# Performance work log

Hardware: AMD Instinct MI355X
Metric: run time of the kernel (lower is better)

Reference implementation:

```python
import jax, jax.numpy as jnp
import numpy as np

BS, T, H = 4, 2048, 512
N_HEAD = 8
D_HEAD = H // N_HEAD  # 64


def setup_inputs() -> dict:
    key = jax.random.key(0)
    k1, k2, k3 = jax.random.split(key, 3)
    x = jax.random.normal(k1, (BS, T, H), dtype=jnp.float32)
    # torch Linear(hidden, (2*n_head+1)*d_head) -> store transposed for x @ W
    w_qkv = jax.random.normal(k2, (H, (2 * N_HEAD + 1) * D_HEAD), dtype=jnp.float32) * (H ** -0.5)
    w_out = jax.random.normal(k3, (D_HEAD, H), dtype=jnp.float32) * (D_HEAD ** -0.5)
    return {"x": x, "w_qkv": w_qkv, "w_out": w_out}


def reference(x, w_qkv, w_out):
    bs, t, h = x.shape
    n_head, d_head = N_HEAD, D_HEAD
    scale = d_head ** -0.5

    qkv = x @ w_qkv  # [bs, t, (2*n_head+1)*d_head]
    q, k, v = jnp.split(qkv, [n_head * d_head, 2 * n_head * d_head], axis=-1)
    q = q.reshape(bs, t, n_head, d_head)
    k = k.reshape(bs, t, n_head, d_head)
    # v stays [bs, t, d_head]: a single V shared across all heads

    # causal mask: -inf strictly above the diagonal
    mask = jnp.triu(jnp.full((t, t), -jnp.inf, dtype=x.dtype), 1)

    # scores: [bs, n_head, t_q, t_k]
    attn_score = jnp.einsum('bqhd,bkhd->bhqk', q, k) * scale + mask
    attn_prob = jax.nn.softmax(attn_score, axis=-1)

    # shared V broadcast over heads: [bs, n_head, t, d_head]
    attn_vec = jnp.einsum('bhqk,bkd->bhqd', attn_prob, v)
    m_attn_vec = jnp.mean(attn_vec, axis=1)  # mean over heads -> [bs, t, d_head]

    out = m_attn_vec @ w_out  # [bs, t, hidden]
    return out, attn_prob
```

## Files before the change

### kernel.cpp

```cpp
#include <hip/hip_runtime.h>

typedef unsigned short u16;
typedef __bf16 bf16x8 __attribute__((ext_vector_type(8)));
typedef float f32x4 __attribute__((ext_vector_type(4)));
static_assert(sizeof(bf16x8) == 16, "bf16x8 must be 16B");

#define MFMA(a, b, c) __builtin_amdgcn_mfma_f32_16x16x32_bf16(a, b, c, 0, 0, 0)

__device__ __forceinline__ u16 f2bf(float f) {
  unsigned u = __float_as_uint(f);
  u += 0x7fffu + ((u >> 16) & 1u);
  return (u16)(u >> 16);
}

__global__ __launch_bounds__(256) void prep_kernel(
    const float* __restrict__ x, const float* __restrict__ wqkv,
    const float* __restrict__ wout, u16* __restrict__ xh,
    u16* __restrict__ wt, u16* __restrict__ wot) {
  int blk = blockIdx.x, tid = threadIdx.x;
  if (blk < 4096) {
    int idx = (blk * 256 + tid) * 4;
    float4 v = *(const float4*)(x + idx);
    ushort4 o;
    o.x = f2bf(v.x); o.y = f2bf(v.y); o.z = f2bf(v.z); o.w = f2bf(v.w);
    *(ushort4*)(xh + idx) = o;
  } else if (blk < 4096 + 2176) {
    int idx = (blk - 4096) * 256 + tid;
    int n = idx >> 9, k = idx & 511;
    float v = wqkv[k * 1088 + n];
    if (n < 512) v *= 0.125f;
    wt[idx] = f2bf(v);
  } else {
    int idx = (blk - 6272) * 256 + tid;
    int n = idx >> 6, d = idx & 63;
    wot[idx] = f2bf(wout[d * 512 + n]);
  }
}

__global__ __launch_bounds__(256) void qkv_gemm_kernel(
    const u16* __restrict__ xh, const u16* __restrict__ wt,
    u16* __restrict__ Qb, u16* __restrict__ Kb, u16* __restrict__ Vt) {
  __shared__ u16 As[128][40];
  __shared__ u16 Bs[64][40];
  const int tid = threadIdx.x;
  const int w = tid >> 6, l = tid & 63, g = l >> 4, c16 = l & 15;
  const int n0 = blockIdx.x * 64;
  const int m0 = blockIdx.y * 128;
  const int arow = tid >> 1, acol = (tid & 1) << 4;
  const int brow = tid >> 2, bcol = (tid & 3) << 3;
  const u16* ap = xh + (size_t)(m0 + arow) * 512 + acol;
  const u16* bp = wt + (size_t)(n0 + brow) * 512 + bcol;
  uint4 pa0 = *(const uint4*)(ap);
  uint4 pa1 = *(const uint4*)(ap + 8);
  uint4 pb0 = *(const uint4*)(bp);
  f32x4 acc[2][4] = {};
  for (int k0 = 0; k0 < 512; k0 += 32) {
    __syncthreads();
    *(uint4*)&As[arow][acol] = pa0;
    *(uint4*)&As[arow][acol + 8] = pa1;
    *(uint4*)&Bs[brow][bcol] = pb0;
    __syncthreads();
    if (k0 + 32 < 512) {
      pa0 = *(const uint4*)(ap + k0 + 32);
      pa1 = *(const uint4*)(ap + k0 + 40);
      pb0 = *(const uint4*)(bp + k0 + 32);
    }
#pragma unroll
    for (int mt = 0; mt < 2; ++mt) {
      bf16x8 a = *(const bf16x8*)&As[w * 32 + mt * 16 + c16][g * 8];
#pragma unroll
      for (int nt = 0; nt < 4; ++nt) {
        bf16x8 b = *(const bf16x8*)&Bs[nt * 16 + c16][g * 8];
        acc[mt][nt] = MFMA(a, b, acc[mt][nt]);
      }
    }
  }
#pragma unroll
  for (int mt = 0; mt < 2; ++mt)
#pragma unroll
    for (int nt = 0; nt < 4; ++nt)
#pragma unroll
      for (int j = 0; j < 4; ++j) {
        u16 bv = f2bf(acc[mt][nt][j]);
        int row = m0 + w * 32 + mt * 16 + g * 4 + j;
        int b = row >> 11, t = row & 2047;
        int col = n0 + nt * 16 + c16;
        if (col < 512) {
          int h = col >> 6, d = col & 63;
          Qb[((size_t)((b << 3) + h) * 2048 + t) * 64 + d] = bv;
        } else if (col < 1024) {
          int cc = col - 512, h = cc >> 6, d = cc & 63;
          Kb[((size_t)((b << 3) + h) * 2048 + t) * 64 + d] = bv;
        } else {
          int d = col - 1024;
          Vt[((size_t)((b << 6) + d)) * 2048 + t] = bv;
        }
      }
}

__global__ __launch_bounds__(256, 4) void attn_kernel(
    const u16* __restrict__ Qb, const u16* __restrict__ Kb,
    const u16* __restrict__ Vt, float* __restrict__ P,
    float* __restrict__ Obuf) {
  __shared__ u16 Ps[64][72];
  const int tid = threadIdx.x;
  const int w = tid >> 6, l = tid & 63, g = l >> 4, c16 = l & 15;
  const int bidx = blockIdx.x;
  const int ii = bidx >> 5, jj = bidx & 31;
  const int qt = ((ii >> 3) & 1) ? (31 - jj) : jj;
  const int bh = ii, b = bh >> 3;

  const u16* qrow = Qb + ((size_t)(bh * 2048 + qt * 64 + w * 16 + c16)) * 64;
  const bf16x8 aq0 = *(const bf16x8*)(qrow + g * 8);
  const bf16x8 aq1 = *(const bf16x8*)(qrow + 32 + g * 8);

  const u16* kb = Kb + ((size_t)bh * 2048) * 64;
  const u16* vb = Vt + ((size_t)(b << 6)) * 2048;

  float lsum = 0.f;

  for (int kt = 0; kt <= qt; ++kt) {
    const u16* kp = kb + (size_t)kt * 4096;
    f32x4 st[4];
    __builtin_amdgcn_s_setprio(1);
#pragma unroll
    for (int nt = 0; nt < 4; ++nt) {
      const u16* kr = kp + (size_t)(nt * 16 + c16) * 64 + g * 8;
      bf16x8 k0 = *(const bf16x8*)(kr);
      bf16x8 k1 = *(const bf16x8*)(kr + 32);
      f32x4 a = {};
      a = MFMA(k0, aq0, a);
      a = MFMA(k1, aq1, a);
      st[nt] = a;
    }
    __builtin_amdgcn_s_setprio(0);
    if (kt == qt) {
#pragma unroll
      for (int nt = 0; nt < 4; ++nt)
#pragma unroll
        for (int j = 0; j < 4; ++j)
          if (nt * 16 + g * 4 + j > w * 16 + c16) st[nt][j] = -3.0e38f;
    }
#pragma unroll
    for (int nt = 0; nt < 4; ++nt)
#pragma unroll
      for (int j = 0; j < 4; ++j) lsum += __expf(st[nt][j]);
  }
  lsum += __shfl_xor(lsum, 16, 64);
  lsum += __shfl_xor(lsum, 32, 64);
  const float rl = 1.0f / lsum;

  f32x4 oacc[4] = {};
  float* prow = P +
      ((size_t)(bh * 2048 + qt * 64 + w * 16 + c16)) * 2048 + g * 4;
  for (int kt = 0; kt <= qt; ++kt) {
    const u16* kp = kb + (size_t)kt * 4096;
    f32x4 st[4];
    __builtin_amdgcn_s_setprio(1);
#pragma unroll
    for (int nt = 0; nt < 4; ++nt) {
      const u16* kr = kp + (size_t)(nt * 16 + c16) * 64 + g * 8;
      bf16x8 k0 = *(const bf16x8*)(kr);
      bf16x8 k1 = *(const bf16x8*)(kr + 32);
      f32x4 a = {};
      a = MFMA(k0, aq0, a);
      a = MFMA(k1, aq1, a);
      st[nt] = a;
    }
    __builtin_amdgcn_s_setprio(0);
    if (kt == qt) {
#pragma unroll
      for (int nt = 0; nt < 4; ++nt)
#pragma unroll
        for (int j = 0; j < 4; ++j)
          if (nt * 16 + g * 4 + j > w * 16 + c16) st[nt][j] = -3.0e38f;
    }
#pragma unroll
    for (int nt = 0; nt < 4; ++nt) {
      f32x4 pv;
#pragma unroll
      for (int j = 0; j < 4; ++j) pv[j] = __expf(st[nt][j]) * rl;
      __builtin_nontemporal_store(
          pv, (f32x4*)(prow + (size_t)kt * 64 + nt * 16));
      unsigned r0, r1;
      asm("v_cvt_pk_bf16_f32 %0, %1, %2" : "=v"(r0) : "v"(pv[0]), "v"(pv[1]));
      asm("v_cvt_pk_bf16_f32 %0, %1, %2" : "=v"(r1) : "v"(pv[2]), "v"(pv[3]));
      uint2 pk; pk.x = r0; pk.y = r1;
      *(uint2*)&Ps[w * 16 + c16][nt * 16 + g * 4] = pk;
    }
    bf16x8 ap0 = *(const bf16x8*)&Ps[w * 16 + c16][g * 8];
    bf16x8 ap1 = *(const bf16x8*)&Ps[w * 16 + c16][32 + g * 8];
    __builtin_amdgcn_s_setprio(1);
#pragma unroll
    for (int nt = 0; nt < 4; ++nt) {
      const u16* vr = vb + (size_t)(nt * 16 + c16) * 2048 + kt * 64 + g * 8;
      bf16x8 v0 = *(const bf16x8*)(vr);
      bf16x8 v1 = *(const bf16x8*)(vr + 32);
      oacc[nt] = MFMA(ap0, v0, oacc[nt]);
      oacc[nt] = MFMA(ap1, v1, oacc[nt]);
    }
    __builtin_amdgcn_s_setprio(0);
  }

  {
    float* obase = Obuf + ((size_t)(bh * 2048 + qt * 64 + w * 16)) * 64;
#pragma unroll
    for (int nt = 0; nt < 4; ++nt)
#pragma unroll
      for (int j = 0; j < 4; ++j)
        obase[(g * 4 + j) * 64 + nt * 16 + c16] = oacc[nt][j];
  }
  {
    int colstart = (qt + 1) * 64;
    int nf4 = (2048 - colstart) >> 2;
    float* base = P + ((size_t)(bh * 2048 + qt * 64)) * 2048;
    f32x4 z = {0.f, 0.f, 0.f, 0.f};
    for (int r = 0; r < 64; ++r) {
      f32x4* rowp = (f32x4*)(base + (size_t)r * 2048 + colstart);
      for (int u = tid; u < nf4; u += 256)
        __builtin_nontemporal_store(z, rowp + u);
    }
  }
}

__global__ __launch_bounds__(256) void mean_kernel(
    const float* __restrict__ Obuf, u16* __restrict__ meanb) {
  int o4 = blockIdx.x * 256 + threadIdx.x;
  int d4 = o4 & 15, t = (o4 >> 4) & 2047, b = o4 >> 15;
  f32x4 acc = {0.f, 0.f, 0.f, 0.f};
#pragma unroll
  for (int h = 0; h < 8; ++h) {
    f32x4 v = *(const f32x4*)(Obuf +
        ((size_t)((b << 3) + h) * 2048 + t) * 64 + d4 * 4);
    acc += v;
  }
  ushort4 o;
  o.x = f2bf(acc[0] * 0.125f); o.y = f2bf(acc[1] * 0.125f);
  o.z = f2bf(acc[2] * 0.125f); o.w = f2bf(acc[3] * 0.125f);
  *(ushort4*)(meanb + (size_t)o4 * 4) = o;
}

__global__ __launch_bounds__(256) void out_gemm_kernel(
    const u16* __restrict__ meanb, const u16* __restrict__ wot,
    float* __restrict__ out) {
  __shared__ u16 As[64][72];
  __shared__ u16 Bs[64][72];
  const int tid = threadIdx.x;
  const int w = tid >> 6, l = tid & 63, g = l >> 4, c16 = l & 15;
  const int n0 = blockIdx.x * 64;
  const int m0 = blockIdx.y * 64;
  const int srow = tid >> 2, scol = (tid & 3) << 4;
  {
    const u16* asrc = meanb + (size_t)(m0 + srow) * 64 + scol;
    *(uint4*)&As[srow][scol] = *(const uint4*)(asrc);
    *(uint4*)&As[srow][scol + 8] = *(const uint4*)(asrc + 8);
    const u16* bsrc = wot + (size_t)(n0 + srow) * 64 + scol;
    *(uint4*)&Bs[srow][scol] = *(const uint4*)(bsrc);
    *(uint4*)&Bs[srow][scol + 8] = *(const uint4*)(bsrc + 8);
  }
  __syncthreads();
  bf16x8 a0 = *(const bf16x8*)&As[w * 16 + c16][g * 8];
  bf16x8 a1 = *(const bf16x8*)&As[w * 16 + c16][32 + g * 8];
  f32x4 acc[4] = {};
#pragma unroll
  for (int nt = 0; nt < 4; ++nt) {
    bf16x8 b0 = *(const bf16x8*)&Bs[nt * 16 + c16][g * 8];
    bf16x8 b1 = *(const bf16x8*)&Bs[nt * 16 + c16][32 + g * 8];
    acc[nt] = MFMA(a0, b0, acc[nt]);
    acc[nt] = MFMA(a1, b1, acc[nt]);
  }
#pragma unroll
  for (int nt = 0; nt < 4; ++nt)
#pragma unroll
    for (int j = 0; j < 4; ++j)
      __builtin_nontemporal_store(
          acc[nt][j],
          out + (size_t)(m0 + w * 16 + g * 4 + j) * 512 + n0 + nt * 16 + c16);
}

extern "C" void kernel_launch(void* const* d_in, const int* in_sizes, int n_in,
                              void* d_out, int out_size, void* d_ws,
                              size_t ws_size, hipStream_t stream) {
  (void)in_sizes; (void)n_in; (void)out_size; (void)ws_size;
  const float* x = (const float*)d_in[0];
  const float* wqkv = (const float*)d_in[1];
  const float* wout = (const float*)d_in[2];
  float* out = (float*)d_out;
  float* P = out + 4194304;

  u16* xh = (u16*)d_ws;
  u16* wt = xh + 4194304;
  u16* wot = wt + 557056;
  u16* Qb = wot + 32768;
  u16* Kb = Qb + 4194304;
  u16* Vt = Kb + 4194304;
  float* Obuf = (float*)(Vt + 524288);
  u16* meanb = xh;

  hipLaunchKernelGGL(prep_kernel, dim3(6400), dim3(256), 0, stream,
                     x, wqkv, wout, xh, wt, wot);
  hipLaunchKernelGGL(qkv_gemm_kernel, dim3(17, 64), dim3(256), 0, stream,
                     xh, wt, Qb, Kb, Vt);
  hipLaunchKernelGGL(attn_kernel, dim3(1024), dim3(256), 0, stream,
                     Qb, Kb, Vt, P, Obuf);
  hipLaunchKernelGGL(mean_kernel, dim3(512), dim3(256), 0, stream,
                     Obuf, meanb);
  hipLaunchKernelGGL(out_gemm_kernel, dim3(8, 128), dim3(256), 0, stream,
                     meanb, wot, out);
}
```

Before: 700.0 us.

## Stage K and V tiles through double-buffered shared memory with register prefetch

Each K and V tile is now loaded once per block into double-buffered LDS, with the next tile prefetched into registers while the current one is used. Before, each of the four waves fetched the full K/V tiles from global memory on its own. The change cuts redundant global/L2 traffic and hides load latency behind the MFMA work. In exchange it adds a __syncthreads per iteration and more LDS and registers. The launch-bounds occupancy hint of 4 is also dropped, which may lower occupancy.

```diff
diff --git a/kernel.cpp b/kernel.cpp
--- a/kernel.cpp
+++ b/kernel.cpp
@@ -98,17 +98,20 @@
       }
 }
 
-__global__ __launch_bounds__(256, 4) void attn_kernel(
+__global__ __launch_bounds__(256) void attn_kernel(
     const u16* __restrict__ Qb, const u16* __restrict__ Kb,
     const u16* __restrict__ Vt, float* __restrict__ P,
     float* __restrict__ Obuf) {
   __shared__ u16 Ps[64][72];
+  __shared__ u16 Ks[2][64][72];
+  __shared__ u16 Vs[2][64][72];
   const int tid = threadIdx.x;
   const int w = tid >> 6, l = tid & 63, g = l >> 4, c16 = l & 15;
   const int bidx = blockIdx.x;
   const int ii = bidx >> 5, jj = bidx & 31;
   const int qt = ((ii >> 3) & 1) ? (31 - jj) : jj;
   const int bh = ii, b = bh >> 3;
+  const int srow = tid >> 2, scol = (tid & 3) << 4;
 
   const u16* qrow = Qb + ((size_t)(bh * 2048 + qt * 64 + w * 16 + c16)) * 64;
   const bf16x8 aq0 = *(const bf16x8*)(qrow + g * 8);
@@ -119,15 +122,24 @@
 
   float lsum = 0.f;
 
+  uint4 ka0 = *(const uint4*)(kb + (size_t)srow * 64 + scol);
+  uint4 ka1 = *(const uint4*)(kb + (size_t)srow * 64 + scol + 8);
   for (int kt = 0; kt <= qt; ++kt) {
-    const u16* kp = kb + (size_t)kt * 4096;
+    const int cur = kt & 1;
+    *(uint4*)&Ks[cur][srow][scol] = ka0;
+    *(uint4*)&Ks[cur][srow][scol + 8] = ka1;
+    if (kt < qt) {
+      const u16* kn = kb + (size_t)((kt + 1) * 64 + srow) * 64 + scol;
+      ka0 = *(const uint4*)(kn);
+      ka1 = *(const uint4*)(kn + 8);
+    }
+    __syncthreads();
     f32x4 st[4];
     __builtin_amdgcn_s_setprio(1);
 #pragma unroll
     for (int nt = 0; nt < 4; ++nt) {
-      const u16* kr = kp + (size_t)(nt * 16 + c16) * 64 + g * 8;
-      bf16x8 k0 = *(const bf16x8*)(kr);
-      bf16x8 k1 = *(const bf16x8*)(kr + 32);
+      bf16x8 k0 = *(const bf16x8*)&Ks[cur][nt * 16 + c16][g * 8];
+      bf16x8 k1 = *(const bf16x8*)&Ks[cur][nt * 16 + c16][32 + g * 8];
       f32x4 a = {};
       a = MFMA(k0, aq0, a);
       a = MFMA(k1, aq1, a);
@@ -150,18 +162,36 @@
   lsum += __shfl_xor(lsum, 32, 64);
   const float rl = 1.0f / lsum;
 
+  __syncthreads();
+
   f32x4 oacc[4] = {};
+  ka0 = *(const uint4*)(kb + (size_t)srow * 64 + scol);
+  ka1 = *(const uint4*)(kb + (size_t)srow * 64 + scol + 8);
+  uint4 va0 = *(const uint4*)(vb + (size_t)srow * 2048 + scol);
+  uint4 va1 = *(const uint4*)(vb + (size_t)srow * 2048 + scol + 8);
   float* prow = P +
       ((size_t)(bh * 2048 + qt * 64 + w * 16 + c16)) * 2048 + g * 4;
   for (int kt = 0; kt <= qt; ++kt) {
-    const u16* kp = kb + (size_t)kt * 4096;
+    const int cur = kt & 1;
+    *(uint4*)&Ks[cur][srow][scol] = ka0;
+    *(uint4*)&Ks[cur][srow][scol + 8] = ka1;
+    *(uint4*)&Vs[cur][srow][scol] = va0;
+    *(uint4*)&Vs[cur][srow][scol + 8] = va1;
+    if (kt < qt) {
+      const u16* kn = kb + (size_t)((kt + 1) * 64 + srow) * 64 + scol;
+      ka0 = *(const uint4*)(kn);
+      ka1 = *(const uint4*)(kn + 8);
+      const u16* vn = vb + (size_t)srow * 2048 + (kt + 1) * 64 + scol;
+      va0 = *(const uint4*)(vn);
+      va1 = *(const uint4*)(vn + 8);
+    }
+    __syncthreads();
     f32x4 st[4];
     __builtin_amdgcn_s_setprio(1);
 #pragma unroll
     for (int nt = 0; nt < 4; ++nt) {
-      const u16* kr = kp + (size_t)(nt * 16 + c16) * 64 + g * 8;
-      bf16x8 k0 = *(const bf16x8*)(kr);
-      bf16x8 k1 = *(const bf16x8*)(kr + 32);
+      bf16x8 k0 = *(const bf16x8*)&Ks[cur][nt * 16 + c16][g * 8];
+      bf16x8 k1 = *(const bf16x8*)&Ks[cur][nt * 16 + c16][32 + g * 8];
       f32x4 a = {};
       a = MFMA(k0, aq0, a);
       a = MFMA(k1, aq1, a);
@@ -193,11 +223,10 @@
     __builtin_amdgcn_s_setprio(1);
 #pragma unroll
     for (int nt = 0; nt < 4; ++nt) {
-      const u16* vr = vb + (size_t)(nt * 16 + c16) * 2048 + kt * 64 + g * 8;
-      bf16x8 v0 = *(const bf16x8*)(vr);
-      bf16x8 v1 = *(const bf16x8*)(vr + 32);
-      oacc[nt] = MFMA(ap0, v0, oacc[nt]);
-      oacc[nt] = MFMA(ap1, v1, oacc[nt]);
+      bf16x8 bv0 = *(const bf16x8*)&Vs[cur][nt * 16 + c16][g * 8];
+      bf16x8 bv1 = *(const bf16x8*)&Vs[cur][nt * 16 + c16][32 + g * 8];
+      oacc[nt] = MFMA(ap0, bv0, oacc[nt]);
+      oacc[nt] = MFMA(ap1, bv1, oacc[nt]);
     }
     __builtin_amdgcn_s_setprio(0);
   }
```

Result: faster. 662.8 us (-5.3%).
